# Optimization experiments

Hardware: AMD Instinct MI355X
Metric: run time of the kernel (lower is better)

Reference implementation:

```python
import jax, jax.numpy as jnp
import numpy as np

EPS = 1e-10


def _make_spd(key, shape):
    # entrywise-nonnegative SPD: B>=0 -> B@B^T has nonnegative entries and is PSD;
    # + c*I keeps it well-conditioned and entrywise nonnegative.
    B = jax.random.uniform(key, shape, dtype=jnp.float32)
    D = jnp.einsum('...ij,...kj->...ik', B, B)
    return D + 0.05 * jnp.eye(3, dtype=jnp.float32)


def setup_inputs() -> dict:
    key = jax.random.key(0)
    k1, k2 = jax.random.split(key)
    shape = (2, 128, 128, 64, 3, 3)
    return {"D1": _make_spd(k1, shape), "D2": _make_spd(k2, shape)}


def _log_spd(D):
    # sanitize like torch.nan_to_num(..., nan=eps, posinf=eps, neginf=eps)
    D = jnp.nan_to_num(D, nan=EPS, posinf=EPS, neginf=EPS)
    D = jnp.abs(D)  # entrywise abs; input is symmetric so abs stays symmetric
    w, V = jnp.linalg.eigh(D)            # [...,3], [...,3,3]
    lw = jnp.log(w + EPS) + EPS
    # V @ diag(lw) @ V^T
    return jnp.einsum('...ij,...j,...kj->...ik', V, lw, V)


def reference(D1, D2):
    diff = _log_spd(D1) - _log_spd(D2)
    return jnp.mean(diff * diff)
```

## Files before the change

kernel.cpp:

```cpp
#include <hip/hip_runtime.h>
#include <math.h>

#define EPS_F 1e-10f

typedef __attribute__((ext_vector_type(4))) float f4;
typedef __attribute__((ext_vector_type(4))) unsigned int u4;
typedef __attribute__((ext_vector_type(2))) float f2;

__device__ __forceinline__ f4 v_fabs(f4 x) {
  u4 u = __builtin_bit_cast(u4, x);
  u &= 0x7fffffffu;
  return __builtin_bit_cast(f4, u);
}
__device__ __forceinline__ f4 v_max(f4 a, f4 b) { return __builtin_elementwise_max(a, b); }
__device__ __forceinline__ f4 v_min(f4 a, f4 b) { return __builtin_elementwise_min(a, b); }
__device__ __forceinline__ f4 v_log(f4 x) {
  f4 r; r.x = __logf(x.x); r.y = __logf(x.y); r.z = __logf(x.z); r.w = __logf(x.w); return r;
}
__device__ __forceinline__ f4 v_rcp(f4 x) {
  f4 r;
  r.x = __builtin_amdgcn_rcpf(x.x); r.y = __builtin_amdgcn_rcpf(x.y);
  r.z = __builtin_amdgcn_rcpf(x.z); r.w = __builtin_amdgcn_rcpf(x.w);
  return r;
}
__device__ __forceinline__ f4 v_sqrt(f4 x) {
  f4 r;
  r.x = __builtin_amdgcn_sqrtf(x.x); r.y = __builtin_amdgcn_sqrtf(x.y);
  r.z = __builtin_amdgcn_sqrtf(x.z); r.w = __builtin_amdgcn_sqrtf(x.w);
  return r;
}
__device__ __forceinline__ f4 v_cos(f4 x) {
  f4 r; r.x = __cosf(x.x); r.y = __cosf(x.y); r.z = __cosf(x.z); r.w = __cosf(x.w); return r;
}

__device__ __forceinline__ f4 v_acos(f4 r) {
  const f4 t = v_fabs(r);
  const f4 s = v_sqrt(1.0f - t);
  f4 p = f4{-0.0012624911f, -0.0012624911f, -0.0012624911f, -0.0012624911f};
  p = p * t +  0.0066700901f;
  p = p * t + -0.0170881256f;
  p = p * t +  0.0308918810f;
  p = p * t + -0.0501743046f;
  p = p * t +  0.0889789874f;
  p = p * t + -0.2145988016f;
  p = p * t +  1.5707963050f;
  const f4 ac = s * p;
  f4 res;
  res.x = (r.x < 0.0f) ? (3.14159265358979f - ac.x) : ac.x;
  res.y = (r.y < 0.0f) ? (3.14159265358979f - ac.y) : ac.y;
  res.z = (r.z < 0.0f) ? (3.14159265358979f - ac.z) : ac.z;
  res.w = (r.w < 0.0f) ? (3.14159265358979f - ac.w) : ac.w;
  return res;
}

__device__ __forceinline__ f2 pair_loss(f4 a00, f4 a01, f4 a02,
                                        f4 a11, f4 a12, f4 a22) {
  a00 = v_fabs(a00); a01 = v_fabs(a01); a02 = v_fabs(a02);
  a11 = v_fabs(a11); a12 = v_fabs(a12); a22 = v_fabs(a22);

  const f4 q   = (a00 + a11 + a22) * (1.0f / 3.0f);
  const f4 b00 = a00 - q, b11 = a11 - q, b22 = a22 - q;
  const f4 p2  = b00 * b00 + b11 * b11 + b22 * b22 +
                 2.0f * (a01 * a01 + a02 * a02 + a12 * a12);

  f4 p = v_sqrt(p2 * (1.0f / 6.0f));
  p = v_max(p, 1e-5f * q + 1e-35f);

  const f4 pinv = v_rcp(p);
  const f4 detB = b00 * (b11 * b22 - a12 * a12)
                - a01 * (a01 * b22 - a12 * a02)
                + a02 * (a01 * a12 - b11 * a02);
  f4 r = detB * 0.5f * pinv * pinv * pinv;
  r = v_min(f4{1.0f, 1.0f, 1.0f, 1.0f}, v_max(f4{-1.0f, -1.0f, -1.0f, -1.0f}, r));
  const f4 phi  = v_acos(r) * (1.0f / 3.0f);
  const f4 twop = 2.0f * p;
  const f4 l1 = q + twop * v_cos(phi);
  const f4 l3 = q + twop * v_cos(phi + 2.0943951023931953f);
  const f4 l2 = 3.0f * q - l1 - l3;

  const f4 s00 = a00 * a00 + a01 * a01 + a02 * a02;
  const f4 s01 = a00 * a01 + a01 * a11 + a02 * a12;
  const f4 s02 = a00 * a02 + a01 * a12 + a02 * a22;
  const f4 s11 = a01 * a01 + a11 * a11 + a12 * a12;
  const f4 s12 = a01 * a02 + a11 * a12 + a12 * a22;
  const f4 s22 = a02 * a02 + a12 * a12 + a22 * a22;

  const f4 g12 = l1 - l2, g23 = l2 - l3;
  f4 alpha, gamma;
  alpha.x = (g12.x >= g23.x) ? l1.x : l3.x;  gamma.x = (g12.x >= g23.x) ? l3.x : l1.x;
  alpha.y = (g12.y >= g23.y) ? l1.y : l3.y;  gamma.y = (g12.y >= g23.y) ? l3.y : l1.y;
  alpha.z = (g12.z >= g23.z) ? l1.z : l3.z;  gamma.z = (g12.z >= g23.z) ? l3.z : l1.z;
  alpha.w = (g12.w >= g23.w) ? l1.w : l3.w;  gamma.w = (g12.w >= g23.w) ? l3.w : l1.w;
  const f4 beta = l2;

  const f4 f_a = v_log(alpha + EPS_F);
  const f4 f_b = v_log(beta  + EPS_F);
  const f4 f_g = v_log(gamma + EPS_F);

  const f4 inv_den_a = v_rcp((alpha - beta) * (alpha - gamma));

  const f4 gap = gamma - beta;
  const f4 ga  = gamma - alpha;
  const f4 agap = v_fabs(gap);
  const f4 thr  = 1e-5f * v_max(v_fabs(beta), v_fabs(gamma));
  const f4 mid  = 0.5f * (beta + gamma) + EPS_F;
  f4 num, den;
  num.x = (agap.x > thr.x) ? (f_g.x - f_b.x) : 1.0f;
  den.x = (agap.x > thr.x) ? (gap.x * ga.x) : (mid.x * ga.x);
  num.y = (agap.y > thr.y) ? (f_g.y - f_b.y) : 1.0f;
  den.y = (agap.y > thr.y) ? (gap.y * ga.y) : (mid.y * ga.y);
  num.z = (agap.z > thr.z) ? (f_g.z - f_b.z) : 1.0f;
  den.z = (agap.z > thr.z) ? (gap.z * ga.z) : (mid.z * ga.z);
  num.w = (agap.w > thr.w) ? (f_g.w - f_b.w) : 1.0f;
  den.w = (agap.w > thr.w) ? (gap.w * ga.w) : (mid.w * ga.w);
  const f4 cg = num * v_rcp(den);
  const f4 wd = (f_a - f_b) * inv_den_a;

  const f4 sbg = beta + gamma, pbg = beta * gamma;
  const f4 sab = alpha + beta, pab = alpha * beta;
  const f4 c2 = wd + cg;
  const f4 c1 = -(wd * sbg + cg * sab);
  const f4 c0 = f_b + wd * pbg + cg * pab;

  const f4 L0 = c2 * s00 + c1 * a00 + c0;
  const f4 L1 = c2 * s01 + c1 * a01;
  const f4 L2 = c2 * s02 + c1 * a02;
  const f4 L3 = c2 * s11 + c1 * a11 + c0;
  const f4 L4 = c2 * s12 + c1 * a12;
  const f4 L5 = c2 * s22 + c1 * a22 + c0;

  const float dA0 = L0.x - L0.y, dB0 = L0.z - L0.w;
  const float dA1 = L1.x - L1.y, dB1 = L1.z - L1.w;
  const float dA2 = L2.x - L2.y, dB2 = L2.z - L2.w;
  const float dA3 = L3.x - L3.y, dB3 = L3.z - L3.w;
  const float dA4 = L4.x - L4.y, dB4 = L4.z - L4.w;
  const float dA5 = L5.x - L5.y, dB5 = L5.z - L5.w;
  f2 out;
  out.x = dA0 * dA0 + dA3 * dA3 + dA5 * dA5 + 2.0f * (dA1 * dA1 + dA2 * dA2 + dA4 * dA4);
  out.y = dB0 * dB0 + dB3 * dB3 + dB5 * dB5 + 2.0f * (dB1 * dB1 + dB2 * dB2 + dB4 * dB4);
  return out;
}

__global__ void __launch_bounds__(256, 4)
leloss_partial(const float* __restrict__ d1, const float* __restrict__ d2,
               float* __restrict__ partial, int nmat) {
  const int nitems = (nmat + 1) >> 1;
  const int stride = gridDim.x * blockDim.x;
  const int tid = threadIdx.x;
  float acc = 0.0f;

  for (int i = blockIdx.x * blockDim.x + tid; i < nitems; i += stride) {
    f4 m00, m01, m02, m11, m12, m22;
    const bool haveB = (2 * i + 1 < nmat);
    if (haveB) {
      const float2* gA = reinterpret_cast<const float2*>(d1) + (size_t)i * 9;
      const float2* gB = reinterpret_cast<const float2*>(d2) + (size_t)i * 9;
      const float2 r0 = gA[0], r1 = gA[1], r2 = gA[2], r4 = gA[4],
                   r5 = gA[5], r6 = gA[6], r7 = gA[7], r8 = gA[8];
      const float2 q0 = gB[0], q1 = gB[1], q2 = gB[2], q4 = gB[4],
                   q5 = gB[5], q6 = gB[6], q7 = gB[7], q8 = gB[8];
      m00 = f4{r0.x, q0.x, r4.y, q4.y};
      m01 = f4{r0.y, q0.y, r5.x, q5.x};
      m02 = f4{r1.x, q1.x, r5.y, q5.y};
      m11 = f4{r2.x, q2.x, r6.y, q6.y};
      m12 = f4{r2.y, q2.y, r7.x, q7.x};
      m22 = f4{r4.x, q4.x, r8.y, q8.y};
    } else {
      const size_t base = (size_t)(2 * i) * 9;
      m00 = f4{d1[base + 0], d2[base + 0], d1[base + 0], d2[base + 0]};
      m01 = f4{d1[base + 1], d2[base + 1], d1[base + 1], d2[base + 1]};
      m02 = f4{d1[base + 2], d2[base + 2], d1[base + 2], d2[base + 2]};
      m11 = f4{d1[base + 4], d2[base + 4], d1[base + 4], d2[base + 4]};
      m12 = f4{d1[base + 5], d2[base + 5], d1[base + 5], d2[base + 5]};
      m22 = f4{d1[base + 8], d2[base + 8], d1[base + 8], d2[base + 8]};
    }
    const f2 l = pair_loss(m00, m01, m02, m11, m12, m22);
    acc += l.x + (haveB ? l.y : 0.0f);
  }

#pragma unroll
  for (int off = 32; off > 0; off >>= 1) acc += __shfl_down(acc, off, 64);

  __shared__ float wsum[4];
  const int lane = tid & 63;
  const int wid  = tid >> 6;
  if (lane == 0) wsum[wid] = acc;
  __syncthreads();
  if (tid == 0) {
    partial[blockIdx.x] = wsum[0] + wsum[1] + wsum[2] + wsum[3];
  }
}

__global__ void __launch_bounds__(256)
leloss_reduce(const float* __restrict__ partial, int n,
              float* __restrict__ out, double inv_count) {
  double s = 0.0;
  for (int i = threadIdx.x; i < n; i += 256) s += (double)partial[i];
#pragma unroll
  for (int off = 32; off > 0; off >>= 1) s += __shfl_down(s, off, 64);

  __shared__ double wsum[4];
  const int lane = threadIdx.x & 63;
  const int wid  = threadIdx.x >> 6;
  if (lane == 0) wsum[wid] = s;
  __syncthreads();
  if (threadIdx.x == 0) {
    const double total = wsum[0] + wsum[1] + wsum[2] + wsum[3];
    out[0] = (float)(total * inv_count);
  }
}

extern "C" void kernel_launch(void* const* d_in, const int* in_sizes, int n_in,
                              void* d_out, int out_size, void* d_ws, size_t ws_size,
                              hipStream_t stream) {
  const float* d1 = (const float*)d_in[0];
  const float* d2 = (const float*)d_in[1];
  float* out = (float*)d_out;
  float* partial = (float*)d_ws;

  const long long nelem = (long long)in_sizes[0];
  const int nmat   = (int)(nelem / 9);
  const int nitems = (nmat + 1) >> 1;
  int nblocks = (nitems + 255) / 256;
  if (nblocks > 2048) nblocks = 2048;

  leloss_partial<<<nblocks, 256, 0, stream>>>(d1, d2, partial, nmat);

  const double inv_count = 1.0 / ((double)nmat * 9.0);
  leloss_reduce<<<1, 256, 0, stream>>>(partial, nblocks, out, inv_count);
}
```

Before: 33.42 us.

## Process two items per thread per iteration and use rsqrt for eigen scale

Each thread now loads and evaluates two independent matrix-pair items per loop iteration, strided by half the thread count, and the grid is halved accordingly. This raises instruction-level parallelism and memory-level parallelism per thread, at the cost of more registers and fewer waves in flight. The sqrt-plus-reciprocal pair is also replaced by a single rsqrt of a clamped p squared, with p recovered by multiplication. The clamp floor is rewritten in squared form, which changes numerics slightly.

Measured after the change: 37.92 us. +13.5%, slower.

```diff
diff --git a/kernel.cpp b/kernel.cpp
--- a/kernel.cpp
+++ b/kernel.cpp
@@ -21,6 +21,12 @@
   f4 r;
   r.x = __builtin_amdgcn_rcpf(x.x); r.y = __builtin_amdgcn_rcpf(x.y);
   r.z = __builtin_amdgcn_rcpf(x.z); r.w = __builtin_amdgcn_rcpf(x.w);
+  return r;
+}
+__device__ __forceinline__ f4 v_rsq(f4 x) {
+  f4 r;
+  r.x = __builtin_amdgcn_rsqf(x.x); r.y = __builtin_amdgcn_rsqf(x.y);
+  r.z = __builtin_amdgcn_rsqf(x.z); r.w = __builtin_amdgcn_rsqf(x.w);
   return r;
 }
 __device__ __forceinline__ f4 v_sqrt(f4 x) {
@@ -63,10 +69,10 @@
   const f4 p2  = b00 * b00 + b11 * b11 + b22 * b22 +
                  2.0f * (a01 * a01 + a02 * a02 + a12 * a12);
 
-  f4 p = v_sqrt(p2 * (1.0f / 6.0f));
-  p = v_max(p, 1e-5f * q + 1e-35f);
-
-  const f4 pinv = v_rcp(p);
+  const f4 p2c  = v_max(p2 * (1.0f / 6.0f), 1e-10f * q * q + 1e-35f);
+  const f4 pinv = v_rsq(p2c);
+  const f4 p    = p2c * pinv;
+
   const f4 detB = b00 * (b11 * b22 - a12 * a12)
                 - a01 * (a01 * b22 - a12 * a02)
                 + a02 * (a01 * a12 - b11 * a02);
@@ -141,41 +147,66 @@
   return out;
 }
 
+__device__ __forceinline__ void load_item(const float* __restrict__ d1,
+                                          const float* __restrict__ d2, int i,
+                                          f4& m00, f4& m01, f4& m02,
+                                          f4& m11, f4& m12, f4& m22) {
+  const float2* gA = reinterpret_cast<const float2*>(d1) + (size_t)i * 9;
+  const float2* gB = reinterpret_cast<const float2*>(d2) + (size_t)i * 9;
+  const float2 r0 = gA[0], r1 = gA[1], r2 = gA[2], r4 = gA[4],
+               r5 = gA[5], r6 = gA[6], r7 = gA[7], r8 = gA[8];
+  const float2 q0 = gB[0], q1 = gB[1], q2 = gB[2], q4 = gB[4],
+               q5 = gB[5], q6 = gB[6], q7 = gB[7], q8 = gB[8];
+  m00 = f4{r0.x, q0.x, r4.y, q4.y};
+  m01 = f4{r0.y, q0.y, r5.x, q5.x};
+  m02 = f4{r1.x, q1.x, r5.y, q5.y};
+  m11 = f4{r2.x, q2.x, r6.y, q6.y};
+  m12 = f4{r2.y, q2.y, r7.x, q7.x};
+  m22 = f4{r4.x, q4.x, r8.y, q8.y};
+}
+
+__device__ __forceinline__ float item_loss_guarded(const float* __restrict__ d1,
+                                                   const float* __restrict__ d2,
+                                                   int i, int nmat) {
+  f4 m00, m01, m02, m11, m12, m22;
+  const bool haveB = (2 * i + 1 < nmat);
+  if (haveB) {
+    load_item(d1, d2, i, m00, m01, m02, m11, m12, m22);
+  } else {
+    const size_t base = (size_t)(2 * i) * 9;
+    m00 = f4{d1[base + 0], d2[base + 0], d1[base + 0], d2[base + 0]};
+    m01 = f4{d1[base + 1], d2[base + 1], d1[base + 1], d2[base + 1]};
+    m02 = f4{d1[base + 2], d2[base + 2], d1[base + 2], d2[base + 2]};
+    m11 = f4{d1[base + 4], d2[base + 4], d1[base + 4], d2[base + 4]};
+    m12 = f4{d1[base + 5], d2[base + 5], d1[base + 5], d2[base + 5]};
+    m22 = f4{d1[base + 8], d2[base + 8], d1[base + 8], d2[base + 8]};
+  }
+  const f2 l = pair_loss(m00, m01, m02, m11, m12, m22);
+  return l.x + (haveB ? l.y : 0.0f);
+}
+
 __global__ void __launch_bounds__(256, 4)
 leloss_partial(const float* __restrict__ d1, const float* __restrict__ d2,
-               float* __restrict__ partial, int nmat) {
+               float* __restrict__ partial, int nmat, int T) {
   const int nitems = (nmat + 1) >> 1;
-  const int stride = gridDim.x * blockDim.x;
   const int tid = threadIdx.x;
+  const int t = blockIdx.x * 256 + tid;
   float acc = 0.0f;
 
-  for (int i = blockIdx.x * blockDim.x + tid; i < nitems; i += stride) {
-    f4 m00, m01, m02, m11, m12, m22;
-    const bool haveB = (2 * i + 1 < nmat);
-    if (haveB) {
-      const float2* gA = reinterpret_cast<const float2*>(d1) + (size_t)i * 9;
-      const float2* gB = reinterpret_cast<const float2*>(d2) + (size_t)i * 9;
-      const float2 r0 = gA[0], r1 = gA[1], r2 = gA[2], r4 = gA[4],
-                   r5 = gA[5], r6 = gA[6], r7 = gA[7], r8 = gA[8];
-      const float2 q0 = gB[0], q1 = gB[1], q2 = gB[2], q4 = gB[4],
-                   q5 = gB[5], q6 = gB[6], q7 = gB[7], q8 = gB[8];
-      m00 = f4{r0.x, q0.x, r4.y, q4.y};
-      m01 = f4{r0.y, q0.y, r5.x, q5.x};
-      m02 = f4{r1.x, q1.x, r5.y, q5.y};
-      m11 = f4{r2.x, q2.x, r6.y, q6.y};
-      m12 = f4{r2.y, q2.y, r7.x, q7.x};
-      m22 = f4{r4.x, q4.x, r8.y, q8.y};
+  for (int i = t; i < nitems; i += 2 * T) {
+    const int i1 = i + T;
+    if (2 * i1 + 1 < nmat) {
+      f4 a00, a01, a02, a11, a12, a22;
+      f4 b00, b01, b02, b11, b12, b22;
+      load_item(d1, d2, i,  a00, a01, a02, a11, a12, a22);
+      load_item(d1, d2, i1, b00, b01, b02, b11, b12, b22);
+      const f2 l0 = pair_loss(a00, a01, a02, a11, a12, a22);
+      const f2 l1 = pair_loss(b00, b01, b02, b11, b12, b22);
+      acc += (l0.x + l0.y) + (l1.x + l1.y);
     } else {
-      const size_t base = (size_t)(2 * i) * 9;
-      m00 = f4{d1[base + 0], d2[base + 0], d1[base + 0], d2[base + 0]};
-      m01 = f4{d1[base + 1], d2[base + 1], d1[base + 1], d2[base + 1]};
-      m02 = f4{d1[base + 2], d2[base + 2], d1[base + 2], d2[base + 2]};
-      m11 = f4{d1[base + 4], d2[base + 4], d1[base + 4], d2[base + 4]};
-      m12 = f4{d1[base + 5], d2[base + 5], d1[base + 5], d2[base + 5]};
-      m22 = f4{d1[base + 8], d2[base + 8], d1[base + 8], d2[base + 8]};
+      acc += item_loss_guarded(d1, d2, i, nmat);
+      if (i1 < nitems) acc += item_loss_guarded(d1, d2, i1, nmat);
     }
-    const f2 l = pair_loss(m00, m01, m02, m11, m12, m22);
-    acc += l.x + (haveB ? l.y : 0.0f);
   }
 
 #pragma unroll
@@ -221,10 +252,11 @@
   const long long nelem = (long long)in_sizes[0];
   const int nmat   = (int)(nelem / 9);
   const int nitems = (nmat + 1) >> 1;
-  int nblocks = (nitems + 255) / 256;
+  int nblocks = (nitems + 511) / 512;
   if (nblocks > 2048) nblocks = 2048;
-
-  leloss_partial<<<nblocks, 256, 0, stream>>>(d1, d2, partial, nmat);
+  const int T = nblocks * 256;
+
+  leloss_partial<<<nblocks, 256, 0, stream>>>(d1, d2, partial, nmat, T);
 
   const double inv_count = 1.0 / ((double)nmat * 9.0);
   leloss_reduce<<<1, 256, 0, stream>>>(partial, nblocks, out, inv_count);
```

## Use one-item-per-thread grid, move odd tail to separate kernel, use rsqrt

Applied to the files above, without the earlier changes.

Drops the grid-stride loop and the 2048-block cap, so each thread handles exactly one pair of matrices with no per-iteration tail branch. The odd leftover matrix is handled by a tiny separate kernel that writes an extra partial, which the final reduce includes. The sqrt+rcp pair is replaced by a single rsqrt and a multiply. The cost is a much larger partial array for the single-block reduce to sum, plus an extra launch when the matrix count is odd.

Result: no change. 33.62 us (+0.6%).

```diff
diff --git a/kernel.cpp b/kernel.cpp
--- a/kernel.cpp
+++ b/kernel.cpp
@@ -21,6 +21,12 @@
   f4 r;
   r.x = __builtin_amdgcn_rcpf(x.x); r.y = __builtin_amdgcn_rcpf(x.y);
   r.z = __builtin_amdgcn_rcpf(x.z); r.w = __builtin_amdgcn_rcpf(x.w);
+  return r;
+}
+__device__ __forceinline__ f4 v_rsq(f4 x) {
+  f4 r;
+  r.x = __builtin_amdgcn_rsqf(x.x); r.y = __builtin_amdgcn_rsqf(x.y);
+  r.z = __builtin_amdgcn_rsqf(x.z); r.w = __builtin_amdgcn_rsqf(x.w);
   return r;
 }
 __device__ __forceinline__ f4 v_sqrt(f4 x) {
@@ -53,8 +59,8 @@
   return res;
 }
 
-__device__ __forceinline__ f2 pair_loss(f4 a00, f4 a01, f4 a02,
-                                        f4 a11, f4 a12, f4 a22) {
+__device__ __forceinline__ float pair_loss(f4 a00, f4 a01, f4 a02,
+                                           f4 a11, f4 a12, f4 a22) {
   a00 = v_fabs(a00); a01 = v_fabs(a01); a02 = v_fabs(a02);
   a11 = v_fabs(a11); a12 = v_fabs(a12); a22 = v_fabs(a22);
 
@@ -63,10 +69,10 @@
   const f4 p2  = b00 * b00 + b11 * b11 + b22 * b22 +
                  2.0f * (a01 * a01 + a02 * a02 + a12 * a12);
 
-  f4 p = v_sqrt(p2 * (1.0f / 6.0f));
-  p = v_max(p, 1e-5f * q + 1e-35f);
-
-  const f4 pinv = v_rcp(p);
+  const f4 p2c  = v_max(p2 * (1.0f / 6.0f), 1e-10f * q * q + 1e-35f);
+  const f4 pinv = v_rsq(p2c);
+  const f4 p    = p2c * pinv;
+
   const f4 detB = b00 * (b11 * b22 - a12 * a12)
                 - a01 * (a01 * b22 - a12 * a02)
                 + a02 * (a01 * a12 - b11 * a02);
@@ -135,47 +141,31 @@
   const float dA3 = L3.x - L3.y, dB3 = L3.z - L3.w;
   const float dA4 = L4.x - L4.y, dB4 = L4.z - L4.w;
   const float dA5 = L5.x - L5.y, dB5 = L5.z - L5.w;
-  f2 out;
-  out.x = dA0 * dA0 + dA3 * dA3 + dA5 * dA5 + 2.0f * (dA1 * dA1 + dA2 * dA2 + dA4 * dA4);
-  out.y = dB0 * dB0 + dB3 * dB3 + dB5 * dB5 + 2.0f * (dB1 * dB1 + dB2 * dB2 + dB4 * dB4);
-  return out;
+  return dA0 * dA0 + dA3 * dA3 + dA5 * dA5 + 2.0f * (dA1 * dA1 + dA2 * dA2 + dA4 * dA4)
+       + dB0 * dB0 + dB3 * dB3 + dB5 * dB5 + 2.0f * (dB1 * dB1 + dB2 * dB2 + dB4 * dB4);
 }
 
 __global__ void __launch_bounds__(256, 4)
 leloss_partial(const float* __restrict__ d1, const float* __restrict__ d2,
-               float* __restrict__ partial, int nmat) {
-  const int nitems = (nmat + 1) >> 1;
-  const int stride = gridDim.x * blockDim.x;
+               float* __restrict__ partial, int nitems) {
   const int tid = threadIdx.x;
+  const int i = blockIdx.x * 256 + tid;
   float acc = 0.0f;
 
-  for (int i = blockIdx.x * blockDim.x + tid; i < nitems; i += stride) {
-    f4 m00, m01, m02, m11, m12, m22;
-    const bool haveB = (2 * i + 1 < nmat);
-    if (haveB) {
-      const float2* gA = reinterpret_cast<const float2*>(d1) + (size_t)i * 9;
-      const float2* gB = reinterpret_cast<const float2*>(d2) + (size_t)i * 9;
-      const float2 r0 = gA[0], r1 = gA[1], r2 = gA[2], r4 = gA[4],
-                   r5 = gA[5], r6 = gA[6], r7 = gA[7], r8 = gA[8];
-      const float2 q0 = gB[0], q1 = gB[1], q2 = gB[2], q4 = gB[4],
-                   q5 = gB[5], q6 = gB[6], q7 = gB[7], q8 = gB[8];
-      m00 = f4{r0.x, q0.x, r4.y, q4.y};
-      m01 = f4{r0.y, q0.y, r5.x, q5.x};
-      m02 = f4{r1.x, q1.x, r5.y, q5.y};
-      m11 = f4{r2.x, q2.x, r6.y, q6.y};
-      m12 = f4{r2.y, q2.y, r7.x, q7.x};
-      m22 = f4{r4.x, q4.x, r8.y, q8.y};
-    } else {
-      const size_t base = (size_t)(2 * i) * 9;
-      m00 = f4{d1[base + 0], d2[base + 0], d1[base + 0], d2[base + 0]};
-      m01 = f4{d1[base + 1], d2[base + 1], d1[base + 1], d2[base + 1]};
-      m02 = f4{d1[base + 2], d2[base + 2], d1[base + 2], d2[base + 2]};
-      m11 = f4{d1[base + 4], d2[base + 4], d1[base + 4], d2[base + 4]};
-      m12 = f4{d1[base + 5], d2[base + 5], d1[base + 5], d2[base + 5]};
-      m22 = f4{d1[base + 8], d2[base + 8], d1[base + 8], d2[base + 8]};
-    }
-    const f2 l = pair_loss(m00, m01, m02, m11, m12, m22);
-    acc += l.x + (haveB ? l.y : 0.0f);
+  if (i < nitems) {
+    const float2* gA = reinterpret_cast<const float2*>(d1) + (size_t)i * 9;
+    const float2* gB = reinterpret_cast<const float2*>(d2) + (size_t)i * 9;
+    const float2 r0 = gA[0], r1 = gA[1], r2 = gA[2], r4 = gA[4],
+                 r5 = gA[5], r6 = gA[6], r7 = gA[7], r8 = gA[8];
+    const float2 q0 = gB[0], q1 = gB[1], q2 = gB[2], q4 = gB[4],
+                 q5 = gB[5], q6 = gB[6], q7 = gB[7], q8 = gB[8];
+    const f4 m00 = f4{r0.x, q0.x, r4.y, q4.y};
+    const f4 m01 = f4{r0.y, q0.y, r5.x, q5.x};
+    const f4 m02 = f4{r1.x, q1.x, r5.y, q5.y};
+    const f4 m11 = f4{r2.x, q2.x, r6.y, q6.y};
+    const f4 m12 = f4{r2.y, q2.y, r7.x, q7.x};
+    const f4 m22 = f4{r4.x, q4.x, r8.y, q8.y};
+    acc = pair_loss(m00, m01, m02, m11, m12, m22);
   }
 
 #pragma unroll
@@ -189,6 +179,18 @@
   if (tid == 0) {
     partial[blockIdx.x] = wsum[0] + wsum[1] + wsum[2] + wsum[3];
   }
+}
+
+__global__ void leloss_tail(const float* __restrict__ d1, const float* __restrict__ d2,
+                            float* __restrict__ partial_slot, int mat_idx) {
+  const size_t base = (size_t)mat_idx * 9;
+  const f4 m00 = f4{d1[base + 0], d2[base + 0], d1[base + 0], d2[base + 0]};
+  const f4 m01 = f4{d1[base + 1], d2[base + 1], d1[base + 1], d2[base + 1]};
+  const f4 m02 = f4{d1[base + 2], d2[base + 2], d1[base + 2], d2[base + 2]};
+  const f4 m11 = f4{d1[base + 4], d2[base + 4], d1[base + 4], d2[base + 4]};
+  const f4 m12 = f4{d1[base + 5], d2[base + 5], d1[base + 5], d2[base + 5]};
+  const f4 m22 = f4{d1[base + 8], d2[base + 8], d1[base + 8], d2[base + 8]};
+  partial_slot[0] = 0.5f * pair_loss(m00, m01, m02, m11, m12, m22);
 }
 
 __global__ void __launch_bounds__(256)
@@ -220,12 +222,17 @@
 
   const long long nelem = (long long)in_sizes[0];
   const int nmat   = (int)(nelem / 9);
-  const int nitems = (nmat + 1) >> 1;
-  int nblocks = (nitems + 255) / 256;
-  if (nblocks > 2048) nblocks = 2048;
-
-  leloss_partial<<<nblocks, 256, 0, stream>>>(d1, d2, partial, nmat);
+  const int nitems = nmat >> 1;
+  const int nblocks = (nitems + 255) / 256;
+
+  leloss_partial<<<nblocks, 256, 0, stream>>>(d1, d2, partial, nitems);
+
+  int npart = nblocks;
+  if (nmat & 1) {
+    leloss_tail<<<1, 1, 0, stream>>>(d1, d2, partial + npart, nmat - 1);
+    ++npart;
+  }
 
   const double inv_count = 1.0 / ((double)nmat * 9.0);
-  leloss_reduce<<<1, 256, 0, stream>>>(partial, nblocks, out, inv_count);
-}
+  leloss_reduce<<<1, 256, 0, stream>>>(partial, npart, out, inv_count);
+}
```
